# Kernel tuning notes

Measured on AMD Instinct MI355X. Metric: run time of the kernel, lower is better.

Reference implementation:

```python
import jax, jax.numpy as jnp
import numpy as np

_N = 2048          # matrix_size (A_sparse.shape[0] in the original)
_NNZ = 32768       # number of factor / pred entries
_LOGCOND_EPS = 1e-12


def setup_inputs() -> dict:
    key = jax.random.key(0)
    k1, k2, k3, k4, k5 = jax.random.split(key, 5)
    pred_values = jax.random.normal(k1, (_NNZ,), dtype=jnp.float32)
    active_scales = jax.random.uniform(k2, (_NNZ,), dtype=jnp.float32) * 0.05
    A_factor = jax.random.normal(k3, (_N, _N), dtype=jnp.float32)
    factor_rows = jax.random.randint(k4, (_NNZ,), 0, _N, dtype=jnp.int32)
    factor_cols = jax.random.randint(k5, (_NNZ,), 0, _N, dtype=jnp.int32)
    return {
        "pred_values": pred_values,
        "active_scales": active_scales,
        "A_factor": A_factor,
        "factor_rows": factor_rows,
        "factor_cols": factor_cols,
    }


def reference(pred_values, active_scales, A_factor, factor_rows, factor_cols):
    n = A_factor.shape[0]
    dt = pred_values.dtype
    # SPD system matrix A (stands in for the original fixed A_sparse)
    A = A_factor @ A_factor.T / jnp.asarray(n, dt) + jnp.eye(n, dtype=dt)
    # Sparse factor L assembled from predicted values (scatter-add, dup-safe),
    # unit diagonal keeps L A L^T well conditioned / SPD.
    L = jnp.eye(n, dtype=dt).at[factor_rows, factor_cols].add(pred_values * active_scales)
    # Preconditioned matrix M = L A L^T (symmetric PSD)
    M = L @ A @ L.T
    M = 0.5 * (M + M.T)
    evals = jnp.linalg.eigvalsh(M)  # ascending
    lam_min = jnp.maximum(evals[0], _LOGCOND_EPS)
    lam_max = jnp.maximum(evals[-1], _LOGCOND_EPS)
    # loss = log(lambda_max) - log(lambda_min) = log condition number
    return jnp.log(lam_max) - jnp.log(lam_min)
```

## Files before the change

### kernel.cpp

```cpp
#include <hip/hip_runtime.h>

#define N2 2048
#define NNZ 32768
#define LK 22
#define NBL 128
#define BINCAP 64

typedef __attribute__((ext_vector_type(8))) _Float16 half8;
typedef __attribute__((ext_vector_type(4))) float f32x4;

#define AGENT __HIP_MEMORY_SCOPE_AGENT
#define AS1C(p) ((const __attribute__((address_space(1))) unsigned int*)(p))
#define AS3(p)  ((__attribute__((address_space(3))) unsigned int*)(p))

__device__ __forceinline__ unsigned short f2h(float f) {
  _Float16 h = (_Float16)f;
  return *(unsigned short*)&h;
}
__device__ __forceinline__ float h2f(unsigned short u) {
  _Float16 h = *(_Float16*)&u;
  return (float)h;
}

__global__ __launch_bounds__(256) void convert_kernel(const float* __restrict__ W,
                                                      unsigned short* __restrict__ Hf,
                                                      unsigned* __restrict__ cnt) {
  if (blockIdx.x < 8) cnt[blockIdx.x * 256 + threadIdx.x] = 0;
  int i4 = blockIdx.x * 256 + threadIdx.x;
  float4 w = ((const float4*)W)[i4];
  ushort4 h;
  h.x = f2h(w.x); h.y = f2h(w.y); h.z = f2h(w.z); h.w = f2h(w.w);
  ((ushort4*)Hf)[i4] = h;
}

__global__ __launch_bounds__(512) void gemm_f16_kernel(const unsigned short* __restrict__ Hf,
                                                       unsigned short* __restrict__ Ah,
                                                       const float* __restrict__ pred,
                                                       const float* __restrict__ scal,
                                                       const int* __restrict__ rows,
                                                       const int* __restrict__ cols,
                                                       unsigned* __restrict__ cnt,
                                                       int* __restrict__ bcol,
                                                       float* __restrict__ bval) {
  const int tid = threadIdx.x;
  if (blockIdx.x < 64) {
    int k = blockIdx.x * 512 + tid;
    int r = rows[k];
    unsigned pos = atomicAdd(&cnt[r], 1u);
    if (pos < BINCAP) {
      bcol[r * BINCAP + pos] = cols[k];
      bval[r * BINCAP + pos] = pred[k] * scal[k];
    }
  }

  int bi, bj;
  bool diag;
  if (blockIdx.x < 32) {
    bi = blockIdx.x; bj = bi >> 1; diag = true;
  } else {
    int idx = blockIdx.x - 32;
    int j = 0;
    while (j < 14 && idx >= (j + 1) * (30 - j)) ++j;
    bj = j;
    bi = 2 * j + 2 + (idx - j * (31 - j));
    diag = false;
  }

  __shared__ unsigned short Xs[2][64 * 32];
  __shared__ unsigned short Ys[2][128 * 32];
  __shared__ float Cred[64 * 132];
  const int w = tid >> 6, lane = tid & 63;
  const int half = w >> 2, wq = w & 3;
  const int row0 = bi * 64, col0 = bj * 128;
  const int m0 = (wq & 1) * 32, n0 = (wq >> 1) * 64;
  f32x4 acc[2][4];
#pragma unroll
  for (int a = 0; a < 2; ++a)
#pragma unroll
    for (int b = 0; b < 4; ++b) acc[a][b] = (f32x4){0.f, 0.f, 0.f, 0.f};
  const int mrow = lane & 15, kseg = (lane >> 4) * 8;
  const int srowX = wq * 16 + (lane >> 2);
  const int srowY = wq * 32 + (lane >> 2);
  const int scol = (lane & 3) * 8;
  const int kbase = half * 1024;

  for (int k0 = 0; k0 < 1024; k0 += 32) {
    __syncthreads();
    __builtin_amdgcn_global_load_lds(
        AS1C(Hf + (size_t)(row0 + srowX) * 2048 + kbase + k0 + scol),
        AS3(Xs[half] + (wq * 16) * 32), 16, 0, 0);
#pragma unroll
    for (int q = 0; q < 2; ++q) {
      __builtin_amdgcn_global_load_lds(
          AS1C(Hf + (size_t)(col0 + srowY + q * 16) * 2048 + kbase + k0 + scol),
          AS3(Ys[half] + (wq * 32 + q * 16) * 32), 16, 0, 0);
    }
    __syncthreads();
    half8 af[2], bf[4];
#pragma unroll
    for (int t = 0; t < 2; ++t)
      af[t] = *(const half8*)(Xs[half] + (m0 + t * 16 + mrow) * 32 + kseg);
#pragma unroll
    for (int t = 0; t < 4; ++t)
      bf[t] = *(const half8*)(Ys[half] + (n0 + t * 16 + mrow) * 32 + kseg);
#pragma unroll
    for (int mt = 0; mt < 2; ++mt)
#pragma unroll
      for (int nt = 0; nt < 4; ++nt)
        acc[mt][nt] = __builtin_amdgcn_mfma_f32_16x16x32_f16(af[mt], bf[nt], acc[mt][nt], 0, 0, 0);
  }
  const int crow = (lane >> 4) * 4, ccol = lane & 15;
  __syncthreads();
  if (half == 1) {
#pragma unroll
    for (int mt = 0; mt < 2; ++mt)
#pragma unroll
      for (int nt = 0; nt < 4; ++nt)
#pragma unroll
        for (int r = 0; r < 4; ++r)
          Cred[(m0 + mt * 16 + crow + r) * 132 + n0 + nt * 16 + ccol] = acc[mt][nt][r];
  }
  __syncthreads();
  if (half == 0) {
    const float invn = 1.0f / 2048.0f;
#pragma unroll
    for (int mt = 0; mt < 2; ++mt)
#pragma unroll
      for (int nt = 0; nt < 4; ++nt) {
        const int gi0 = row0 + m0 + mt * 16 + crow;
        const int gj = col0 + n0 + nt * 16 + ccol;
        size_t base = (size_t)gi0 * 2048 + gj;
#pragma unroll
        for (int r = 0; r < 4; ++r) {
          const int li = (m0 + mt * 16 + crow + r) * 132 + n0 + nt * 16 + ccol;
          float val = (acc[mt][nt][r] + Cred[li]) * invn +
                      ((gi0 + r == gj) ? 1.0f : 0.0f);
          Ah[base + (size_t)r * 2048] = f2h(val);
          if (!diag) Cred[li] = val;
        }
      }
  }
  if (!diag) {
    __syncthreads();
    const int orow = tid >> 2;
    const int cseg = (tid & 3) * 16;
    unsigned short mv[16];
#pragma unroll
    for (int k = 0; k < 16; ++k)
      mv[k] = f2h(Cred[(cseg + k) * 132 + orow]);
    uint4* dst = (uint4*)(Ah + (size_t)(col0 + orow) * 2048 + row0 + cseg);
    dst[0] = *(uint4*)&mv[0];
    dst[1] = *(uint4*)&mv[8];
  }
}

__global__ __launch_bounds__(256) void gatherF_kernel(const unsigned* __restrict__ cnt,
                                                      const int* __restrict__ bcol,
                                                      const float* __restrict__ bval,
                                                      const unsigned short* __restrict__ Ah,
                                                      unsigned short* __restrict__ F) {
  const int r = blockIdx.x, tid = threadIdx.x;
  __shared__ int scol_[BINCAP];
  __shared__ float sval_[BINCAP];
  const unsigned ne = min(cnt[r], (unsigned)BINCAP);
  if (tid < ne) {
    scol_[tid] = bcol[r * BINCAP + tid];
    sval_[tid] = bval[r * BINCAP + tid];
  }
  __syncthreads();
  float acc[8] = {0.f, 0.f, 0.f, 0.f, 0.f, 0.f, 0.f, 0.f};
  unsigned e = 0;
  for (; e + 4 <= ne; e += 4) {
    uint4 q0 = *(const uint4*)(Ah + (size_t)scol_[e + 0] * 2048 + tid * 8);
    uint4 q1 = *(const uint4*)(Ah + (size_t)scol_[e + 1] * 2048 + tid * 8);
    uint4 q2 = *(const uint4*)(Ah + (size_t)scol_[e + 2] * 2048 + tid * 8);
    uint4 q3 = *(const uint4*)(Ah + (size_t)scol_[e + 3] * 2048 + tid * 8);
    half8 h0 = *(half8*)&q0, h1 = *(half8*)&q1, h2 = *(half8*)&q2, h3 = *(half8*)&q3;
    const float v0 = sval_[e], v1 = sval_[e + 1], v2 = sval_[e + 2], v3 = sval_[e + 3];
#pragma unroll
    for (int k = 0; k < 8; ++k) {
      acc[k] += v0 * (float)h0[k];
      acc[k] += v1 * (float)h1[k];
      acc[k] += v2 * (float)h2[k];
      acc[k] += v3 * (float)h3[k];
    }
  }
  for (; e < ne; ++e) {
    uint4 q = *(const uint4*)(Ah + (size_t)scol_[e] * 2048 + tid * 8);
    half8 hv = *(half8*)&q;
    const float v = sval_[e];
#pragma unroll
    for (int k = 0; k < 8; ++k) acc[k] += v * (float)hv[k];
  }
  unsigned short o[8];
#pragma unroll
  for (int k = 0; k < 8; ++k) o[k] = f2h(acc[k]);
  *(uint4*)(F + (size_t)r * 2048 + tid * 8) = *(uint4*)o;
}

__global__ __launch_bounds__(256) void transpose_kernel(const unsigned short* __restrict__ F,
                                                        unsigned short* __restrict__ Ft) {
  __shared__ unsigned short T2[64][66];
  const int bi = blockIdx.x, bj = blockIdx.y;
  const int c8 = (threadIdx.x & 7) * 8;
  const int rr = threadIdx.x >> 3;
#pragma unroll
  for (int h = 0; h < 2; ++h) {
    const int r = rr + h * 32;
    uint4 raw = *(const uint4*)(F + (size_t)(bj * 64 + r) * 2048 + bi * 64 + c8);
    const unsigned* pw = (const unsigned*)&raw;
#pragma unroll
    for (int i = 0; i < 4; ++i)
      *(unsigned*)&T2[r][c8 + i * 2] = pw[i];
  }
  __syncthreads();
#pragma unroll
  for (int h = 0; h < 2; ++h) {
    const int r = rr + h * 32;
    unsigned short tv[8];
#pragma unroll
    for (int k = 0; k < 8; ++k) tv[k] = T2[c8 + k][r];
    *(uint4*)(Ft + (size_t)(bi * 64 + r) * 2048 + bj * 64 + c8) = *(uint4*)tv;
  }
}

__global__ __launch_bounds__(256) void finalM_kernel(const unsigned* __restrict__ cnt,
                                                     const int* __restrict__ bcol,
                                                     const float* __restrict__ bval,
                                                     const unsigned short* __restrict__ Ah,
                                                     const unsigned short* __restrict__ F,
                                                     const unsigned short* __restrict__ Ft,
                                                     float* __restrict__ M) {
  const int r = blockIdx.x, tid = threadIdx.x;
  __shared__ int scol_[BINCAP];
  __shared__ float sval_[BINCAP];
  const unsigned ne = min(cnt[r], (unsigned)BINCAP);
  if (tid < ne) {
    scol_[tid] = bcol[r * BINCAP + tid];
    sval_[tid] = bval[r * BINCAP + tid];
  }
  __syncthreads();
  float acc[8] = {0.f, 0.f, 0.f, 0.f, 0.f, 0.f, 0.f, 0.f};
  unsigned e = 0;
  for (; e + 4 <= ne; e += 4) {
    uint4 q0 = *(const uint4*)(Ft + (size_t)scol_[e + 0] * 2048 + tid * 8);
    uint4 q1 = *(const uint4*)(Ft + (size_t)scol_[e + 1] * 2048 + tid * 8);
    uint4 q2 = *(const uint4*)(Ft + (size_t)scol_[e + 2] * 2048 + tid * 8);
    uint4 q3 = *(const uint4*)(Ft + (size_t)scol_[e + 3] * 2048 + tid * 8);
    half8 h0 = *(half8*)&q0, h1 = *(half8*)&q1, h2 = *(half8*)&q2, h3 = *(half8*)&q3;
    const float v0 = sval_[e], v1 = sval_[e + 1], v2 = sval_[e + 2], v3 = sval_[e + 3];
#pragma unroll
    for (int k = 0; k < 8; ++k) {
      acc[k] += v0 * (float)h0[k];
      acc[k] += v1 * (float)h1[k];
      acc[k] += v2 * (float)h2[k];
      acc[k] += v3 * (float)h3[k];
    }
  }
  for (; e < ne; ++e) {
    uint4 q = *(const uint4*)(Ft + (size_t)scol_[e] * 2048 + tid * 8);
    half8 hv = *(half8*)&q;
    const float v = sval_[e];
#pragma unroll
    for (int k = 0; k < 8; ++k) acc[k] += v * (float)hv[k];
  }
  const size_t off = (size_t)r * 2048 + tid * 8;
  uint4 ra = *(const uint4*)(Ah + off);
  uint4 rf = *(const uint4*)(F + off);
  uint4 rt = *(const uint4*)(Ft + off);
  half8 ha = *(half8*)&ra, hf = *(half8*)&rf, ht = *(half8*)&rt;
  float out[8];
#pragma unroll
  for (int k = 0; k < 8; ++k)
    out[k] = (float)ha[k] + ((float)hf[k] + (float)ht[k]) + acc[k];
  float4* Mo = (float4*)(M + off);
  Mo[0] = (float4){out[0], out[1], out[2], out[3]};
  Mo[1] = (float4){out[4], out[5], out[6], out[7]};
}

__device__ __forceinline__ float block_sum8(float v, float* red) {
#pragma unroll
  for (int off = 32; off; off >>= 1) v += __shfl_down(v, off);
  if ((threadIdx.x & 63) == 0) red[threadIdx.x >> 6] = v;
  __syncthreads();
  float r = ((red[0] + red[1]) + (red[2] + red[3])) +
            ((red[4] + red[5]) + (red[6] + red[7]));
  __syncthreads();
  return r;
}

__global__ __launch_bounds__(512) void lanczos_kernel(const float* __restrict__ M,
                                                      unsigned long long* __restrict__ Z0,
                                                      unsigned long long* __restrict__ Z1,
                                                      float* __restrict__ out) {
  const int tid = threadIdx.x, b = blockIdx.x;
  const int wave = tid >> 6, lane = tid & 63;
  __shared__ __align__(16) float Mlds[16 * 2048];
  __shared__ __align__(16) float VA[2048];
  __shared__ __align__(16) float VB[2048];
  __shared__ float red[8];
  __shared__ float al[LK + 2], b2[LK + 2];
  __shared__ float bnds[2], res[2];

  const float* Mblk = M + (size_t)b * 16 * 2048;
#pragma unroll
  for (int q = 0; q < 16; ++q)
    __builtin_amdgcn_global_load_lds(AS1C(Mblk + wave * 4096 + q * 256 + lane * 4),
                                     AS3(Mlds + wave * 4096 + q * 256), 16, 0, 0);

  float pv[4];
  float part = 0.f;
#pragma unroll
  for (int t = 0; t < 4; ++t) {
    int i = t * 512 + tid;
    unsigned u = (unsigned)i * 2654435761u;
    u ^= u >> 16; u *= 2246822519u; u ^= u >> 13;
    float rv = (float)(u >> 8) * (2.f / 16777216.f) - 1.f;
    pv[t] = rv;
    part += rv * rv;
  }
  float nrm = block_sum8(part, red);
  float innm = rsqrtf(nrm);
#pragma unroll
  for (int t = 0; t < 4; ++t) {
    int i = t * 512 + tid;
    VA[i] = pv[t] * innm;
    VB[i] = 0.f;
  }
  __syncthreads();

  float* Vcur = VA;
  float* Vprev = VB;
  float beta_prev = 0.f;

  for (int j = 1; j <= LK; ++j) {
    unsigned long long* Z = (j & 1) ? Z0 : Z1;
#pragma unroll
    for (int rr = 0; rr < 2; ++rr) {
      const int r = b * 16 + wave * 2 + rr;
      const float4* Mr = (const float4*)(Mlds + (wave * 2 + rr) * 2048);
      float s = 0.f;
#pragma unroll
      for (int t = 0; t < 8; ++t) {
        int idx = t * 64 + lane;
        float4 m4 = Mr[idx];
        float4 v4 = ((const float4*)Vcur)[idx];
        s += m4.x * v4.x + m4.y * v4.y + m4.z * v4.z + m4.w * v4.w;
      }
#pragma unroll
      for (int off = 32; off; off >>= 1) s += __shfl_down(s, off);
      if (lane == 0) {
        float zv = s - beta_prev * Vprev[r];
        unsigned long long pk = ((unsigned long long)(unsigned)j << 32) |
                                (unsigned long long)(unsigned)__float_as_uint(zv);
        __hip_atomic_store(&Z[r], pk, __ATOMIC_RELAXED, AGENT);
      }
    }

    float va[4];
#pragma unroll
    for (int t = 0; t < 4; ++t) va[t] = Vcur[t * 512 + tid];

    unsigned long long w4[4];
    int rounds = 0;
    for (;;) {
      bool ok = true;
#pragma unroll
      for (int t = 0; t < 4; ++t) {
        w4[t] = __hip_atomic_load(&Z[t * 512 + tid], __ATOMIC_RELAXED, AGENT);
        ok &= ((unsigned)(w4[t] >> 32) == (unsigned)j);
      }
      if (ok) break;
      if (rounds == 1)      __builtin_amdgcn_s_sleep(1);
      else if (rounds == 2) __builtin_amdgcn_s_sleep(2);
      else if (rounds >= 3) __builtin_amdgcn_s_sleep(8);
      ++rounds;
    }
    float za[4];
    float pa = 0.f;
#pragma unroll
    for (int t = 0; t < 4; ++t) {
      za[t] = __uint_as_float((unsigned)w4[t]);
      pa += za[t] * va[t];
    }
    float alpha = block_sum8(pa, red);
    float pb = 0.f;
#pragma unroll
    for (int t = 0; t < 4; ++t) {
      float rsd = za[t] - alpha * va[t];
      pb += rsd * rsd;
    }
    float beta2 = block_sum8(pb, red);
    float beta = sqrtf(fmaxf(beta2, 1e-30f));
    float invb = 1.f / beta;
    if (tid == 0) { al[j] = alpha; b2[j] = beta2; }
#pragma unroll
    for (int t = 0; t < 4; ++t) {
      int i = t * 512 + tid;
      Vprev[i] = (za[t] - alpha * va[t]) * invb;
    }
    float* tmp = Vprev; Vprev = Vcur; Vcur = tmp;
    beta_prev = beta;
    __syncthreads();
  }

  if (b == 0) {
    if (tid == 0) {
      float lo = 1e30f, hi = -1e30f;
      for (int i = 1; i <= LK; ++i) {
        float bl = (i > 1) ? sqrtf(b2[i - 1]) : 0.f;
        float br = (i < LK) ? sqrtf(b2[i]) : 0.f;
        lo = fminf(lo, al[i] - bl - br);
        hi = fmaxf(hi, al[i] + bl + br);
      }
      bnds[0] = lo; bnds[1] = hi;
    }
    __syncthreads();
    if (wave < 2) {
      const int tcount = (wave == 0) ? 1 : LK;
      float lo = bnds[0], hi = bnds[1];
      for (int round = 0; round < 4; ++round) {
        float x = lo + (hi - lo) * (float)(lane + 1) * (1.f / 65.f);
        int cnt = 0;
        float d = al[1] - x;
        if (fabsf(d) < 1e-25f) d = -1e-25f;
        if (d < 0.f) cnt++;
        for (int i = 2; i <= LK; ++i) {
          d = (al[i] - x) - b2[i - 1] / d;
          if (fabsf(d) < 1e-25f) d = -1e-25f;
          if (d < 0.f) cnt++;
        }
        bool ab = (cnt >= tcount);
        float cand_hi = ab ? x : hi;
        float cand_lo = ab ? lo : x;
#pragma unroll
        for (int off = 32; off; off >>= 1) {
          cand_hi = fminf(cand_hi, __shfl_down(cand_hi, off));
          cand_lo = fmaxf(cand_lo, __shfl_down(cand_lo, off));
        }
        cand_hi = __shfl(cand_hi, 0);
        cand_lo = __shfl(cand_lo, 0);
        hi = cand_hi;
        lo = fminf(cand_lo, hi);
      }
      if (lane == 0) res[wave] = 0.5f * (lo + hi);
    }
    __syncthreads();
    if (tid == 0) {
      float lmin = fmaxf(res[0], 1e-12f);
      float lmax = fmaxf(res[1], 1e-12f);
      out[0] = logf(lmax) - logf(lmin);
    }
  }
}

extern "C" void kernel_launch(void* const* d_in, const int* in_sizes, int n_in,
                              void* d_out, int out_size, void* d_ws, size_t ws_size,
                              hipStream_t stream) {
  const float* pred = (const float*)d_in[0];
  const float* scal = (const float*)d_in[1];
  const float* W    = (const float*)d_in[2];
  const int*   rows = (const int*)d_in[3];
  const int*   cols = (const int*)d_in[4];
  float* out = (float*)d_out;

  char* ws = (char*)d_ws;
  const size_t MB = 1024 * 1024;
  unsigned short* Hf = (unsigned short*)(ws);
  unsigned short* Ah = (unsigned short*)(ws + 8 * MB);
  unsigned short* F  = (unsigned short*)(ws + 16 * MB);
  unsigned short* Ft = (unsigned short*)(ws);
  float* M = (float*)(ws + 24 * MB);
  char* ctrl = ws + 40 * MB;
  unsigned* cnt  = (unsigned*)(ctrl);
  int*      bcol = (int*)(ctrl + 8192);
  float*    bval = (float*)(ctrl + 8192 + 524288);
  unsigned long long* Z0 = (unsigned long long*)(ctrl + 8192 + 1048576);
  unsigned long long* Z1 = (unsigned long long*)(ctrl + 8192 + 1048576 + 16384);

  convert_kernel<<<4096, 256, 0, stream>>>(W, Hf, cnt);
  gemm_f16_kernel<<<272, 512, 0, stream>>>(Hf, Ah, pred, scal, rows, cols, cnt, bcol, bval);

  gatherF_kernel<<<2048, 256, 0, stream>>>(cnt, bcol, bval, Ah, F);
  transpose_kernel<<<dim3(32, 32), 256, 0, stream>>>(F, Ft);
  finalM_kernel<<<2048, 256, 0, stream>>>(cnt, bcol, bval, Ah, F, Ft, M);

  lanczos_kernel<<<NBL, 512, 0, stream>>>(M, Z0, Z1, out);
}
```

Baseline: 255.4 us.

## Double-buffer GEMM LDS tiles and unroll sparse gathers by eight

The f16 GEMM kernel now keeps two LDS buffers per K-half. It issues the next tile's global_load_lds before computing on the current one, which removes one barrier per iteration and overlaps loads with MFMA work. Cred is aliased onto the same shared memory to keep the LDS footprint bounded. The gatherF and finalM sparse row loops add an 8-wide unrolled stage so more independent global loads are in flight per thread. Without an explicit vmcnt wait before the barrier, the async LDS loads may race with the reads. Deeper unrolling also raises register pressure.

```diff
diff --git a/kernel.cpp b/kernel.cpp
--- a/kernel.cpp
+++ b/kernel.cpp
@@ -31,6 +31,21 @@
   ushort4 h;
   h.x = f2h(w.x); h.y = f2h(w.y); h.z = f2h(w.z); h.w = f2h(w.w);
   ((ushort4*)Hf)[i4] = h;
+}
+
+__device__ __forceinline__ void stage_tiles(const unsigned short* __restrict__ Hf,
+                                            unsigned short* Xb, unsigned short* Yb,
+                                            int row0, int col0, int kk,
+                                            int srowX, int srowY, int scol, int wq) {
+  __builtin_amdgcn_global_load_lds(
+      AS1C(Hf + (size_t)(row0 + srowX) * 2048 + kk + scol),
+      AS3(Xb + (wq * 16) * 32), 16, 0, 0);
+#pragma unroll
+  for (int q = 0; q < 2; ++q) {
+    __builtin_amdgcn_global_load_lds(
+        AS1C(Hf + (size_t)(col0 + srowY + q * 16) * 2048 + kk + scol),
+        AS3(Yb + (wq * 32 + q * 16) * 32), 16, 0, 0);
+  }
 }
 
 __global__ __launch_bounds__(512) void gemm_f16_kernel(const unsigned short* __restrict__ Hf,
@@ -66,9 +81,11 @@
     diag = false;
   }
 
-  __shared__ unsigned short Xs[2][64 * 32];
-  __shared__ unsigned short Ys[2][128 * 32];
-  __shared__ float Cred[64 * 132];
+  __shared__ __align__(16) char smem[49152];
+  unsigned short* Xs = (unsigned short*)smem;
+  unsigned short* Ys = (unsigned short*)(smem + 16384);
+  float* Cred = (float*)smem;
+
   const int w = tid >> 6, lane = tid & 63;
   const int half = w >> 2, wq = w & 3;
   const int row0 = bi * 64, col0 = bj * 128;
@@ -84,25 +101,25 @@
   const int scol = (lane & 3) * 8;
   const int kbase = half * 1024;
 
-  for (int k0 = 0; k0 < 1024; k0 += 32) {
+  stage_tiles(Hf, Xs + (half * 2 + 0) * 2048, Ys + (half * 2 + 0) * 4096,
+              row0, col0, kbase, srowX, srowY, scol, wq);
+
+  for (int t = 0; t < 32; ++t) {
+    const int cur = t & 1;
     __syncthreads();
-    __builtin_amdgcn_global_load_lds(
-        AS1C(Hf + (size_t)(row0 + srowX) * 2048 + kbase + k0 + scol),
-        AS3(Xs[half] + (wq * 16) * 32), 16, 0, 0);
-#pragma unroll
-    for (int q = 0; q < 2; ++q) {
-      __builtin_amdgcn_global_load_lds(
-          AS1C(Hf + (size_t)(col0 + srowY + q * 16) * 2048 + kbase + k0 + scol),
-          AS3(Ys[half] + (wq * 32 + q * 16) * 32), 16, 0, 0);
-    }
-    __syncthreads();
+    if (t < 31)
+      stage_tiles(Hf, Xs + (half * 2 + (cur ^ 1)) * 2048,
+                  Ys + (half * 2 + (cur ^ 1)) * 4096,
+                  row0, col0, kbase + (t + 1) * 32, srowX, srowY, scol, wq);
+    const unsigned short* Xb = Xs + (half * 2 + cur) * 2048;
+    const unsigned short* Yb = Ys + (half * 2 + cur) * 4096;
     half8 af[2], bf[4];
 #pragma unroll
-    for (int t = 0; t < 2; ++t)
-      af[t] = *(const half8*)(Xs[half] + (m0 + t * 16 + mrow) * 32 + kseg);
-#pragma unroll
-    for (int t = 0; t < 4; ++t)
-      bf[t] = *(const half8*)(Ys[half] + (n0 + t * 16 + mrow) * 32 + kseg);
+    for (int q = 0; q < 2; ++q)
+      af[q] = *(const half8*)(Xb + (m0 + q * 16 + mrow) * 32 + kseg);
+#pragma unroll
+    for (int q = 0; q < 4; ++q)
+      bf[q] = *(const half8*)(Yb + (n0 + q * 16 + mrow) * 32 + kseg);
 #pragma unroll
     for (int mt = 0; mt < 2; ++mt)
 #pragma unroll
@@ -170,24 +187,35 @@
   __syncthreads();
   float acc[8] = {0.f, 0.f, 0.f, 0.f, 0.f, 0.f, 0.f, 0.f};
   unsigned e = 0;
+  for (; e + 8 <= ne; e += 8) {
+    uint4 q[8];
+#pragma unroll
+    for (int u = 0; u < 8; ++u)
+      q[u] = *(const uint4*)(Ah + (size_t)scol_[e + u] * 2048 + tid * 8);
+#pragma unroll
+    for (int u = 0; u < 8; ++u) {
+      half8 hv = *(half8*)&q[u];
+      const float v = sval_[e + u];
+#pragma unroll
+      for (int k = 0; k < 8; ++k) acc[k] += v * (float)hv[k];
+    }
+  }
   for (; e + 4 <= ne; e += 4) {
-    uint4 q0 = *(const uint4*)(Ah + (size_t)scol_[e + 0] * 2048 + tid * 8);
-    uint4 q1 = *(const uint4*)(Ah + (size_t)scol_[e + 1] * 2048 + tid * 8);
-    uint4 q2 = *(const uint4*)(Ah + (size_t)scol_[e + 2] * 2048 + tid * 8);
-    uint4 q3 = *(const uint4*)(Ah + (size_t)scol_[e + 3] * 2048 + tid * 8);
-    half8 h0 = *(half8*)&q0, h1 = *(half8*)&q1, h2 = *(half8*)&q2, h3 = *(half8*)&q3;
-    const float v0 = sval_[e], v1 = sval_[e + 1], v2 = sval_[e + 2], v3 = sval_[e + 3];
-#pragma unroll
-    for (int k = 0; k < 8; ++k) {
-      acc[k] += v0 * (float)h0[k];
-      acc[k] += v1 * (float)h1[k];
-      acc[k] += v2 * (float)h2[k];
-      acc[k] += v3 * (float)h3[k];
+    uint4 q[4];
+#pragma unroll
+    for (int u = 0; u < 4; ++u)
+      q[u] = *(const uint4*)(Ah + (size_t)scol_[e + u] * 2048 + tid * 8);
+#pragma unroll
+    for (int u = 0; u < 4; ++u) {
+      half8 hv = *(half8*)&q[u];
+      const float v = sval_[e + u];
+#pragma unroll
+      for (int k = 0; k < 8; ++k) acc[k] += v * (float)hv[k];
     }
   }
   for (; e < ne; ++e) {
-    uint4 q = *(const uint4*)(Ah + (size_t)scol_[e] * 2048 + tid * 8);
-    half8 hv = *(half8*)&q;
+    uint4 qq = *(const uint4*)(Ah + (size_t)scol_[e] * 2048 + tid * 8);
+    half8 hv = *(half8*)&qq;
     const float v = sval_[e];
 #pragma unroll
     for (int k = 0; k < 8; ++k) acc[k] += v * (float)hv[k];
@@ -242,24 +270,35 @@
   __syncthreads();
   float acc[8] = {0.f, 0.f, 0.f, 0.f, 0.f, 0.f, 0.f, 0.f};
   unsigned e = 0;
+  for (; e + 8 <= ne; e += 8) {
+    uint4 q[8];
+#pragma unroll
+    for (int u = 0; u < 8; ++u)
+      q[u] = *(const uint4*)(Ft + (size_t)scol_[e + u] * 2048 + tid * 8);
+#pragma unroll
+    for (int u = 0; u < 8; ++u) {
+      half8 hv = *(half8*)&q[u];
+      const float v = sval_[e + u];
+#pragma unroll
+      for (int k = 0; k < 8; ++k) acc[k] += v * (float)hv[k];
+    }
+  }
   for (; e + 4 <= ne; e += 4) {
-    uint4 q0 = *(const uint4*)(Ft + (size_t)scol_[e + 0] * 2048 + tid * 8);
-    uint4 q1 = *(const uint4*)(Ft + (size_t)scol_[e + 1] * 2048 + tid * 8);
-    uint4 q2 = *(const uint4*)(Ft + (size_t)scol_[e + 2] * 2048 + tid * 8);
-    uint4 q3 = *(const uint4*)(Ft + (size_t)scol_[e + 3] * 2048 + tid * 8);
-    half8 h0 = *(half8*)&q0, h1 = *(half8*)&q1, h2 = *(half8*)&q2, h3 = *(half8*)&q3;
-    const float v0 = sval_[e], v1 = sval_[e + 1], v2 = sval_[e + 2], v3 = sval_[e + 3];
-#pragma unroll
-    for (int k = 0; k < 8; ++k) {
-      acc[k] += v0 * (float)h0[k];
-      acc[k] += v1 * (float)h1[k];
-      acc[k] += v2 * (float)h2[k];
-      acc[k] += v3 * (float)h3[k];
+    uint4 q[4];
+#pragma unroll
+    for (int u = 0; u < 4; ++u)
+      q[u] = *(const uint4*)(Ft + (size_t)scol_[e + u] * 2048 + tid * 8);
+#pragma unroll
+    for (int u = 0; u < 4; ++u) {
+      half8 hv = *(half8*)&q[u];
+      const float v = sval_[e + u];
+#pragma unroll
+      for (int k = 0; k < 8; ++k) acc[k] += v * (float)hv[k];
     }
   }
   for (; e < ne; ++e) {
-    uint4 q = *(const uint4*)(Ft + (size_t)scol_[e] * 2048 + tid * 8);
-    half8 hv = *(half8*)&q;
+    uint4 qq = *(const uint4*)(Ft + (size_t)scol_[e] * 2048 + tid * 8);
+    half8 hv = *(half8*)&qq;
     const float v = sval_[e];
 #pragma unroll
     for (int k = 0; k < 8; ++k) acc[k] += v * (float)hv[k];
```

New measurement: 251.2 us. Within noise of the previous version (-1.7%).
